# Kernel optimization log

Measured on AMD Instinct MI355X. Metric: run time of the kernel, lower is better.

## Reference

```python
import jax, jax.numpy as jnp
import numpy as np

N_NODES = 50000
N_EDGES = 1600000
NFEAT = 512
HIDDEN = 128
NUM_CLASSES = 40
DROPOUT = 0.5


def setup_inputs() -> dict:
    key = jax.random.key(0)
    ks = jax.random.split(key, 8)
    x = jax.random.normal(ks[0], (N_NODES, NFEAT), dtype=jnp.float32)
    edge_row = jax.random.randint(ks[1], (N_EDGES,), 0, N_NODES, dtype=jnp.int32)
    edge_col = jax.random.randint(ks[2], (N_EDGES,), 0, N_NODES, dtype=jnp.int32)
    edge_vals = jax.random.uniform(ks[3], (N_EDGES,), dtype=jnp.float32)
    # uniform(-stdv, stdv) init as in reset_parameters
    stdv1 = 1.0 / np.sqrt(HIDDEN)
    stdv2 = 1.0 / np.sqrt(NUM_CLASSES)
    W1 = jax.random.uniform(ks[4], (NFEAT, HIDDEN), dtype=jnp.float32, minval=-stdv1, maxval=stdv1)
    b1 = jax.random.uniform(ks[5], (HIDDEN,), dtype=jnp.float32, minval=-stdv1, maxval=stdv1)
    W2 = jax.random.uniform(ks[6], (HIDDEN, NUM_CLASSES), dtype=jnp.float32, minval=-stdv2, maxval=stdv2)
    b2 = jax.random.uniform(ks[7], (NUM_CLASSES,), dtype=jnp.float32, minval=-stdv2, maxval=stdv2)
    return {"x": x, "edge_row": edge_row, "edge_col": edge_col, "edge_vals": edge_vals,
            "W1": W1, "b1": b1, "W2": W2, "b2": b2}


def _spmm(edge_row, edge_col, edge_vals, support):
    # out[i] = sum_{e: row[e]==i} vals[e] * support[col[e]]  (sparse adj @ support)
    msgs = support[edge_col] * edge_vals[:, None]  # [E, F]
    return jax.ops.segment_sum(msgs, edge_row, num_segments=N_NODES)


def _dropout(x, rate, key):
    keep = 1.0 - rate
    mask = jax.random.bernoulli(key, keep, x.shape)
    return jnp.where(mask, x / keep, jnp.zeros((), x.dtype))


def reference(x, edge_row, edge_col, edge_vals, W1, b1, W2, b2):
    # layer 1: GCN conv + bias + relu + dropout (training=True)
    h = _spmm(edge_row, edge_col, edge_vals, x @ W1) + b1  # [N, H]
    h = jax.nn.relu(h)
    h = _dropout(h, DROPOUT, jax.random.key(42))
    # layer 2: GCN conv + bias + relu
    out = _spmm(edge_row, edge_col, edge_vals, h @ W2) + b2  # [N, C]
    return jax.nn.relu(out)
```

## Files before the change

### kernel.cpp

```cpp
#include <hip/hip_runtime.h>
#include <hip/hip_bf16.h>

#define N_NODES 50000
#define N_EDGES 1600000
#define NFEAT   512
#define HIDDEN  128
#define NCLASS  40

#define NBUCK 391
#define ROWS_PER_BUCKET 128
#define BUCK_PAD 4608

#define W1T_BLOCKS 256
#define GEMM1_BLOCKS 391
#define PART_T 4096
#define PART_BLOCKS 391

#define FUSED_LDS 37944

typedef short short8 __attribute__((ext_vector_type(8)));
typedef float f32x4  __attribute__((ext_vector_type(4)));

__device__ __forceinline__ unsigned short f2bu(float f) {
  __hip_bfloat16 h = __float2bfloat16(f);
  return *reinterpret_cast<unsigned short*>(&h);
}

__device__ __forceinline__ unsigned rotl32(unsigned x, int n) {
  return (x << n) | (x >> (32 - n));
}

__device__ __forceinline__ unsigned threefry_bits(unsigned x1) {
  unsigned x0 = 0u;
  const unsigned ks0 = 0u, ks1 = 42u, ks2 = 0x1BD11BDAu ^ 42u;
  x0 += ks0; x1 += ks1;
#define TFR(r) { x0 += x1; x1 = rotl32(x1, (r)); x1 ^= x0; }
  TFR(13) TFR(15) TFR(26) TFR(6)
  x0 += ks1; x1 += ks2 + 1u;
  TFR(17) TFR(29) TFR(16) TFR(24)
  x0 += ks2; x1 += ks0 + 2u;
  TFR(13) TFR(15) TFR(26) TFR(6)
  x0 += ks0; x1 += ks1 + 3u;
  TFR(17) TFR(29) TFR(16) TFR(24)
  x0 += ks1; x1 += ks2 + 4u;
  TFR(13) TFR(15) TFR(26) TFR(6)
  x0 += ks2; x1 += ks0 + 5u;
#undef TFR
  return x0 ^ x1;
}

__global__ __launch_bounds__(256) void init_w1t_kernel(
    const float* __restrict__ W1, unsigned short* __restrict__ W1T,
    int* __restrict__ gcur) {
  if (blockIdx.x < W1T_BLOCKS) {
    int id = blockIdx.x * 256 + threadIdx.x;
    int n = id & 127, k = id >> 7;
    W1T[n * NFEAT + k] = f2bu(W1[k * HIDDEN + n]);
  } else {
    int b = threadIdx.x;
    if (b < NBUCK) gcur[b] = b * BUCK_PAD;
    b += 256;
    if (b < NBUCK) gcur[b] = b * BUCK_PAD;
  }
}

__device__ __forceinline__ void gemm1_body(
    int bid, char* smem, const float* __restrict__ x,
    const unsigned short* __restrict__ W1T,
    unsigned short* __restrict__ support) {
  short8* As = (short8*)smem;
  short8* Bs = (short8*)(smem + 8192);
  const int t = threadIdx.x;
  const int lane = t & 63;
  const int w = t >> 6;
  const int quad = lane >> 4;
  const int l15 = lane & 15;
  const int node_base = bid * 128;
  const int mbase = (w >> 1) * 64;
  const int nbase = (w & 1) * 64;

  f32x4 acc[4][4] = {};

  for (int k0 = 0; k0 < NFEAT; k0 += 32) {
#pragma unroll
    for (int i = 0; i < 2; i++) {
      int lin = i * 256 + t;
      int n = lin >> 2, q = lin & 3;
      int row = node_base + n;
      if (row >= N_NODES) row = N_NODES - 1;
      const float* src = &x[(size_t)row * NFEAT + k0 + q * 8];
      float4 a = *(const float4*)src;
      float4 b = *(const float4*)(src + 4);
      short8 p;
      p[0] = (short)f2bu(a.x); p[1] = (short)f2bu(a.y);
      p[2] = (short)f2bu(a.z); p[3] = (short)f2bu(a.w);
      p[4] = (short)f2bu(b.x); p[5] = (short)f2bu(b.y);
      p[6] = (short)f2bu(b.z); p[7] = (short)f2bu(b.w);
      As[q * 128 + n] = p;
      Bs[q * 128 + n] = *(const short8*)&W1T[(size_t)n * NFEAT + k0 + q * 8];
    }
    __syncthreads();
    short8 af[4], bfr[4];
#pragma unroll
    for (int mt = 0; mt < 4; mt++)
      af[mt] = As[quad * 128 + mbase + mt * 16 + l15];
#pragma unroll
    for (int nt = 0; nt < 4; nt++)
      bfr[nt] = Bs[quad * 128 + nbase + nt * 16 + l15];
#pragma unroll
    for (int mt = 0; mt < 4; mt++)
#pragma unroll
      for (int nt = 0; nt < 4; nt++)
        acc[mt][nt] = __builtin_amdgcn_mfma_f32_16x16x32_bf16(
            af[mt], bfr[nt], acc[mt][nt], 0, 0, 0);
    __syncthreads();
  }

#pragma unroll
  for (int mt = 0; mt < 4; mt++)
#pragma unroll
    for (int nt = 0; nt < 4; nt++)
#pragma unroll
      for (int r = 0; r < 4; r++) {
        int row = node_base + mbase + mt * 16 + quad * 4 + r;
        int col = nbase + nt * 16 + l15;
        if (row < N_NODES)
          support[(size_t)row * HIDDEN + col] = f2bu(acc[mt][nt][r]);
      }
}

__device__ __forceinline__ void partition_body(
    int bid, char* smem, const int* __restrict__ erow,
    const int* __restrict__ ecol, const float* __restrict__ evals,
    int* __restrict__ gcur, uint2* __restrict__ eb) {
  uint2* sorted = (uint2*)smem;
  int* cnt   = (int*)(smem + 32768);
  int* shift = (int*)(smem + 32768 + 1564);
  int* ssc   = (int*)(smem + 32768 + 3128);
  const int t = threadIdx.x;
  const int base = bid * PART_T;

  if (t < NBUCK) cnt[t] = 0;
  if (t + 256 < NBUCK) cnt[t + 256] = 0;
  __syncthreads();

  uint2 er[16];
  unsigned short loc[16];
#pragma unroll
  for (int k = 0; k < 16; k++) {
    int idx = base + k * 256 + t;
    if (idx < N_EDGES) {
      int r = erow[idx];
      er[k].y = (unsigned)r;
      er[k].x = (unsigned)ecol[idx] | ((unsigned)f2bu(evals[idx]) << 16);
      loc[k] = (unsigned short)atomicAdd(&cnt[r >> 7], 1);
    } else {
      er[k].y = 0xffffffffu;
    }
  }
  __syncthreads();

  ssc[t] = (t < NBUCK) ? cnt[t] : 0;
  ssc[t + 256] = (t + 256 < NBUCK) ? cnt[t + 256] : 0;
  __syncthreads();
#pragma unroll
  for (int off = 1; off < 512; off <<= 1) {
    int v0 = (t >= off) ? ssc[t - off] : 0;
    int v1 = ssc[t + 256 - off];
    __syncthreads();
    ssc[t] += v0; ssc[t + 256] += v1;
    __syncthreads();
  }

  for (int b = t; b < NBUCK; b += 256) {
    int c = cnt[b];
    if (c > 0) {
      int lb = ssc[b] - c;
      int gb = atomicAdd(&gcur[b], c);
      shift[b] = gb - lb;
    }
  }
#pragma unroll
  for (int k = 0; k < 16; k++) {
    if (er[k].y != 0xffffffffu) {
      int b = (int)(er[k].y >> 7);
      sorted[ssc[b] - cnt[b] + (int)loc[k]] = er[k];
    }
  }
  __syncthreads();

  const int total = ssc[NBUCK - 1];
  for (int i = t; i < total; i += 256) {
    uint2 e = sorted[i];
    eb[shift[e.y >> 7] + i] = e;
  }
}

__global__ __launch_bounds__(256) void part_gemm1_kernel(
    const int* __restrict__ erow, const int* __restrict__ ecol,
    const float* __restrict__ evals, int* __restrict__ gcur,
    uint2* __restrict__ eb, const float* __restrict__ x,
    const unsigned short* __restrict__ W1T,
    unsigned short* __restrict__ support) {
  __shared__ char smem[FUSED_LDS];
  if (blockIdx.x < PART_BLOCKS)
    partition_body(blockIdx.x, smem, erow, ecol, evals, gcur, eb);
  else
    gemm1_body(blockIdx.x - PART_BLOCKS, smem, x, W1T, support);
}

__global__ __launch_bounds__(512) void csr_build_kernel(
    const uint2* __restrict__ eb, const int* __restrict__ gcur,
    unsigned* __restrict__ csr, int* __restrict__ rowptr,
    int* __restrict__ rowend) {
  __shared__ int cnt[ROWS_PER_BUCKET];
  __shared__ int sc[ROWS_PER_BUCKET];
  __shared__ int cur[ROWS_PER_BUCKET];
  const int t = threadIdx.x;
  const int b = blockIdx.x;
  if (t < ROWS_PER_BUCKET) cnt[t] = 0;
  __syncthreads();
  const int beg = b * BUCK_PAD;
  const int end = gcur[b];
  for (int j = beg + t; j < end; j += 512)
    atomicAdd(&cnt[eb[j].y & 127u], 1);
  __syncthreads();
  if (t < ROWS_PER_BUCKET) sc[t] = cnt[t];
  __syncthreads();
#pragma unroll
  for (int off = 1; off < ROWS_PER_BUCKET; off <<= 1) {
    int v = 0;
    if (t >= off && t < ROWS_PER_BUCKET) v = sc[t - off];
    __syncthreads();
    if (t < ROWS_PER_BUCKET) sc[t] += v;
    __syncthreads();
  }
  if (t < ROWS_PER_BUCKET) {
    int excl = sc[t] - cnt[t];
    cur[t] = excl;
    int row = b * ROWS_PER_BUCKET + t;
    if (row < N_NODES) {
      rowptr[row] = beg + excl;
      rowend[row] = beg + sc[t];
    }
  }
  __syncthreads();
  for (int j = beg + t; j < end; j += 512) {
    uint2 e = eb[j];
    int p = atomicAdd(&cur[e.y & 127u], 1);
    csr[beg + p] = e.x;
  }
}

__global__ __launch_bounds__(256) void spmm1_fused(
    const unsigned* __restrict__ csr, const int* __restrict__ rowptr,
    const int* __restrict__ rowend,
    const unsigned* __restrict__ sup,
    const float* __restrict__ b1, const float* __restrict__ W2,
    unsigned* __restrict__ h2u) {
  __shared__ float Ws[HIDDEN * NCLASS];
  __shared__ unsigned hrow[4][64];
  const int t = threadIdx.x;
#pragma unroll
  for (int i = 0; i < 20; i++) Ws[i * 256 + t] = W2[i * 256 + t];
  __syncthreads();

  const int row = blockIdx.x * 4 + (t >> 6);
  const int wv = t >> 6;
  const int lane = t & 63;
  const int beg = __builtin_amdgcn_readfirstlane(rowptr[row]);
  const int end = __builtin_amdgcn_readfirstlane(rowend[row]);
  float ax = 0.f, ay = 0.f;
  int j = beg;
  for (; j + 15 < end; j += 16) {
    unsigned ps[16];
#pragma unroll
    for (int k = 0; k < 16; k++)
      ps[k] = __builtin_amdgcn_readfirstlane(csr[j + k]);
    unsigned u[16];
#pragma unroll
    for (int k = 0; k < 16; k++)
      u[k] = sup[(size_t)(ps[k] & 0xffffu) * 64 + lane];
#pragma unroll
    for (int k = 0; k < 16; k++) {
      float v = __uint_as_float(ps[k] & 0xffff0000u);
      ax += v * __uint_as_float(u[k] << 16);
      ay += v * __uint_as_float(u[k] & 0xffff0000u);
    }
  }
  for (; j + 7 < end; j += 8) {
    unsigned ps[8];
#pragma unroll
    for (int k = 0; k < 8; k++)
      ps[k] = __builtin_amdgcn_readfirstlane(csr[j + k]);
    unsigned u[8];
#pragma unroll
    for (int k = 0; k < 8; k++)
      u[k] = sup[(size_t)(ps[k] & 0xffffu) * 64 + lane];
#pragma unroll
    for (int k = 0; k < 8; k++) {
      float v = __uint_as_float(ps[k] & 0xffff0000u);
      ax += v * __uint_as_float(u[k] << 16);
      ay += v * __uint_as_float(u[k] & 0xffff0000u);
    }
  }
  for (; j + 1 < end; j += 2) {
    unsigned p0 = __builtin_amdgcn_readfirstlane(csr[j]);
    unsigned p1 = __builtin_amdgcn_readfirstlane(csr[j + 1]);
    unsigned u0 = sup[(size_t)(p0 & 0xffffu) * 64 + lane];
    unsigned u1 = sup[(size_t)(p1 & 0xffffu) * 64 + lane];
    float v0 = __uint_as_float(p0 & 0xffff0000u);
    float v1 = __uint_as_float(p1 & 0xffff0000u);
    ax += v0 * __uint_as_float(u0 << 16) + v1 * __uint_as_float(u1 << 16);
    ay += v0 * __uint_as_float(u0 & 0xffff0000u) +
          v1 * __uint_as_float(u1 & 0xffff0000u);
  }
  if (j < end) {
    unsigned p0 = __builtin_amdgcn_readfirstlane(csr[j]);
    unsigned u0 = sup[(size_t)(p0 & 0xffffu) * 64 + lane];
    float v0 = __uint_as_float(p0 & 0xffff0000u);
    ax += v0 * __uint_as_float(u0 << 16);
    ay += v0 * __uint_as_float(u0 & 0xffff0000u);
  }
  const unsigned i0 = (unsigned)row * HIDDEN + lane * 2;
  float vx = fmaxf(ax + b1[lane * 2], 0.f);
  float vy = fmaxf(ay + b1[lane * 2 + 1], 0.f);
  vx = (threefry_bits(i0) >> 31) ? 0.f : 2.f * vx;
  vy = (threefry_bits(i0 + 1) >> 31) ? 0.f : 2.f * vy;
  hrow[wv][lane] = (unsigned)f2bu(vx) | ((unsigned)f2bu(vy) << 16);
  __syncthreads();

  float accv = 0.f;
  if (lane < NCLASS) {
#pragma unroll 8
    for (int i = 0; i < 64; i++) {
      unsigned u = hrow[wv][i];
      float h0 = __uint_as_float(u << 16);
      float h1 = __uint_as_float(u & 0xffff0000u);
      accv += h0 * Ws[(2 * i) * NCLASS + lane] +
              h1 * Ws[(2 * i + 1) * NCLASS + lane];
    }
    float other = __shfl_xor(accv, 1);
    if (!(lane & 1))
      h2u[(unsigned)row * 20 + (lane >> 1)] =
          (unsigned)f2bu(accv) | ((unsigned)f2bu(other) << 16);
  }
}

__global__ __launch_bounds__(256) void spmm2_fused(
    const unsigned* __restrict__ csr, const int* __restrict__ rowptr,
    const int* __restrict__ rowend,
    const unsigned* __restrict__ h2u,
    const float* __restrict__ b2, float* __restrict__ out) {
  const int row = blockIdx.x * 4 + (threadIdx.x >> 6);
  const int lane = threadIdx.x & 63;
  const int half = lane >> 5;
  const int il = lane & 31;
  const unsigned ilc = (il < 20) ? (unsigned)il : 19u;
  const int beg = rowptr[row], end = rowend[row];
  float ax = 0.f, ay = 0.f;
  int j = beg + half;
  for (; j + 6 < end; j += 8) {
    unsigned p[4], u[4];
#pragma unroll
    for (int k = 0; k < 4; k++) p[k] = csr[j + 2 * k];
#pragma unroll
    for (int k = 0; k < 4; k++) u[k] = h2u[(p[k] & 0xffffu) * 20 + ilc];
#pragma unroll
    for (int k = 0; k < 4; k++) {
      float v = __uint_as_float(p[k] & 0xffff0000u);
      ax += v * __uint_as_float(u[k] << 16);
      ay += v * __uint_as_float(u[k] & 0xffff0000u);
    }
  }
  for (; j + 2 < end; j += 4) {
    unsigned p0 = csr[j];
    unsigned p1 = csr[j + 2];
    unsigned u0 = h2u[(p0 & 0xffffu) * 20 + ilc];
    unsigned u1 = h2u[(p1 & 0xffffu) * 20 + ilc];
    float v0 = __uint_as_float(p0 & 0xffff0000u);
    float v1 = __uint_as_float(p1 & 0xffff0000u);
    ax += v0 * __uint_as_float(u0 << 16) + v1 * __uint_as_float(u1 << 16);
    ay += v0 * __uint_as_float(u0 & 0xffff0000u) +
          v1 * __uint_as_float(u1 & 0xffff0000u);
  }
  for (; j < end; j += 2) {
    unsigned p0 = csr[j];
    unsigned u0 = h2u[(p0 & 0xffffu) * 20 + ilc];
    float v0 = __uint_as_float(p0 & 0xffff0000u);
    ax += v0 * __uint_as_float(u0 << 16);
    ay += v0 * __uint_as_float(u0 & 0xffff0000u);
  }
  ax += __shfl_xor(ax, 32);
  ay += __shfl_xor(ay, 32);
  if (half == 0 && il < 20) {
    float2 r;
    r.x = fmaxf(ax + b2[il * 2], 0.f);
    r.y = fmaxf(ay + b2[il * 2 + 1], 0.f);
    *(float2*)&out[(unsigned)row * NCLASS + il * 2] = r;
  }
}

extern "C" void kernel_launch(void* const* d_in, const int* in_sizes, int n_in,
                              void* d_out, int out_size, void* d_ws,
                              size_t ws_size, hipStream_t stream) {
  const float* x     = (const float*)d_in[0];
  const int*   erow  = (const int*)d_in[1];
  const int*   ecol  = (const int*)d_in[2];
  const float* evals = (const float*)d_in[3];
  const float* W1    = (const float*)d_in[4];
  const float* b1    = (const float*)d_in[5];
  const float* W2    = (const float*)d_in[6];
  const float* b2    = (const float*)d_in[7];
  float* out = (float*)d_out;

  char* base = (char*)d_ws;
  unsigned short* support = (unsigned short*)base;
  uint2*          eb  = (uint2*)(base + 12800000);
  unsigned*       h2  = (unsigned*)(base + 27213824);
  unsigned short* W1T = (unsigned short*)(base + 31213824);
  unsigned*       csr = (unsigned*)(base + 31344896);
  int* rowptr = (int*)(base + 38551808);
  int* rowend = (int*)(base + 38751808);
  int* gcur   = (int*)(base + 38951808);

  init_w1t_kernel<<<W1T_BLOCKS + 1, 256, 0, stream>>>(W1, W1T, gcur);
  part_gemm1_kernel<<<PART_BLOCKS + GEMM1_BLOCKS, 256, 0, stream>>>(
      erow, ecol, evals, gcur, eb, x, W1T, support);
  csr_build_kernel<<<NBUCK, 512, 0, stream>>>(eb, gcur, csr, rowptr, rowend);
  spmm1_fused<<<N_NODES / 4, 256, 0, stream>>>(
      csr, rowptr, rowend, (const unsigned*)support, b1, W2, h2);
  spmm2_fused<<<N_NODES / 4, 256, 0, stream>>>(csr, rowptr, rowend,
                                               (const unsigned*)h2, b2, out);
}
```

Baseline: 313.3 us.

## Co-schedule GEMM1 with CSR build instead of partition; unpack hidden row to fp32

The edge partition step now runs as its own kernel, and GEMM1 blocks are fused with the CSR build kernel instead, which runs at 256 threads per block. Pairing GEMM1 with the lighter CSR build lowers that kernel's LDS footprint to 16KB, which may raise occupancy for the MFMA GEMM. The partition no longer overlaps with anything. Separately, spmm1 stores the dropped-out hidden row as fp32 in LDS and fully unrolls the W2 dot product, removing per-iteration bf16 unpacking.

```diff
diff --git a/kernel.cpp b/kernel.cpp
--- a/kernel.cpp
+++ b/kernel.cpp
@@ -15,8 +15,6 @@
 #define GEMM1_BLOCKS 391
 #define PART_T 4096
 #define PART_BLOCKS 391
-
-#define FUSED_LDS 37944
 
 typedef short short8 __attribute__((ext_vector_type(8)));
 typedef float f32x4  __attribute__((ext_vector_type(4)));
@@ -64,6 +62,73 @@
   }
 }
 
+__global__ __launch_bounds__(256) void partition_kernel(
+    const int* __restrict__ erow, const int* __restrict__ ecol,
+    const float* __restrict__ evals, int* __restrict__ gcur,
+    uint2* __restrict__ eb) {
+  __shared__ uint2 sorted[PART_T];
+  __shared__ int cnt[NBUCK];
+  __shared__ int shift[NBUCK];
+  __shared__ int ssc[512];
+  const int t = threadIdx.x;
+  const int base = blockIdx.x * PART_T;
+
+  if (t < NBUCK) cnt[t] = 0;
+  if (t + 256 < NBUCK) cnt[t + 256] = 0;
+  __syncthreads();
+
+  uint2 er[16];
+  unsigned short loc[16];
+#pragma unroll
+  for (int k = 0; k < 16; k++) {
+    int idx = base + k * 256 + t;
+    if (idx < N_EDGES) {
+      int r = erow[idx];
+      er[k].y = (unsigned)r;
+      er[k].x = (unsigned)ecol[idx] | ((unsigned)f2bu(evals[idx]) << 16);
+      loc[k] = (unsigned short)atomicAdd(&cnt[r >> 7], 1);
+    } else {
+      er[k].y = 0xffffffffu;
+    }
+  }
+  __syncthreads();
+
+  ssc[t] = (t < NBUCK) ? cnt[t] : 0;
+  ssc[t + 256] = (t + 256 < NBUCK) ? cnt[t + 256] : 0;
+  __syncthreads();
+#pragma unroll
+  for (int off = 1; off < 512; off <<= 1) {
+    int v0 = (t >= off) ? ssc[t - off] : 0;
+    int v1 = ssc[t + 256 - off];
+    __syncthreads();
+    ssc[t] += v0; ssc[t + 256] += v1;
+    __syncthreads();
+  }
+
+  for (int b = t; b < NBUCK; b += 256) {
+    int c = cnt[b];
+    if (c > 0) {
+      int lb = ssc[b] - c;
+      int gb = atomicAdd(&gcur[b], c);
+      shift[b] = gb - lb;
+    }
+  }
+#pragma unroll
+  for (int k = 0; k < 16; k++) {
+    if (er[k].y != 0xffffffffu) {
+      int b = (int)(er[k].y >> 7);
+      sorted[ssc[b] - cnt[b] + (int)loc[k]] = er[k];
+    }
+  }
+  __syncthreads();
+
+  const int total = ssc[NBUCK - 1];
+  for (int i = t; i < total; i += 256) {
+    uint2 e = sorted[i];
+    eb[shift[e.y >> 7] + i] = e;
+  }
+}
+
 __device__ __forceinline__ void gemm1_body(
     int bid, char* smem, const float* __restrict__ x,
     const unsigned short* __restrict__ W1T,
@@ -129,100 +194,19 @@
       }
 }
 
-__device__ __forceinline__ void partition_body(
-    int bid, char* smem, const int* __restrict__ erow,
-    const int* __restrict__ ecol, const float* __restrict__ evals,
-    int* __restrict__ gcur, uint2* __restrict__ eb) {
-  uint2* sorted = (uint2*)smem;
-  int* cnt   = (int*)(smem + 32768);
-  int* shift = (int*)(smem + 32768 + 1564);
-  int* ssc   = (int*)(smem + 32768 + 3128);
+__device__ __forceinline__ void csr_body(
+    int b, char* smem, const uint2* __restrict__ eb,
+    const int* __restrict__ gcur, unsigned* __restrict__ csr,
+    int* __restrict__ rowptr, int* __restrict__ rowend) {
+  int* cnt = (int*)smem;
+  int* sc  = (int*)(smem + 512);
+  int* cur = (int*)(smem + 1024);
   const int t = threadIdx.x;
-  const int base = bid * PART_T;
-
-  if (t < NBUCK) cnt[t] = 0;
-  if (t + 256 < NBUCK) cnt[t + 256] = 0;
-  __syncthreads();
-
-  uint2 er[16];
-  unsigned short loc[16];
-#pragma unroll
-  for (int k = 0; k < 16; k++) {
-    int idx = base + k * 256 + t;
-    if (idx < N_EDGES) {
-      int r = erow[idx];
-      er[k].y = (unsigned)r;
-      er[k].x = (unsigned)ecol[idx] | ((unsigned)f2bu(evals[idx]) << 16);
-      loc[k] = (unsigned short)atomicAdd(&cnt[r >> 7], 1);
-    } else {
-      er[k].y = 0xffffffffu;
-    }
-  }
-  __syncthreads();
-
-  ssc[t] = (t < NBUCK) ? cnt[t] : 0;
-  ssc[t + 256] = (t + 256 < NBUCK) ? cnt[t + 256] : 0;
-  __syncthreads();
-#pragma unroll
-  for (int off = 1; off < 512; off <<= 1) {
-    int v0 = (t >= off) ? ssc[t - off] : 0;
-    int v1 = ssc[t + 256 - off];
-    __syncthreads();
-    ssc[t] += v0; ssc[t + 256] += v1;
-    __syncthreads();
-  }
-
-  for (int b = t; b < NBUCK; b += 256) {
-    int c = cnt[b];
-    if (c > 0) {
-      int lb = ssc[b] - c;
-      int gb = atomicAdd(&gcur[b], c);
-      shift[b] = gb - lb;
-    }
-  }
-#pragma unroll
-  for (int k = 0; k < 16; k++) {
-    if (er[k].y != 0xffffffffu) {
-      int b = (int)(er[k].y >> 7);
-      sorted[ssc[b] - cnt[b] + (int)loc[k]] = er[k];
-    }
-  }
-  __syncthreads();
-
-  const int total = ssc[NBUCK - 1];
-  for (int i = t; i < total; i += 256) {
-    uint2 e = sorted[i];
-    eb[shift[e.y >> 7] + i] = e;
-  }
-}
-
-__global__ __launch_bounds__(256) void part_gemm1_kernel(
-    const int* __restrict__ erow, const int* __restrict__ ecol,
-    const float* __restrict__ evals, int* __restrict__ gcur,
-    uint2* __restrict__ eb, const float* __restrict__ x,
-    const unsigned short* __restrict__ W1T,
-    unsigned short* __restrict__ support) {
-  __shared__ char smem[FUSED_LDS];
-  if (blockIdx.x < PART_BLOCKS)
-    partition_body(blockIdx.x, smem, erow, ecol, evals, gcur, eb);
-  else
-    gemm1_body(blockIdx.x - PART_BLOCKS, smem, x, W1T, support);
-}
-
-__global__ __launch_bounds__(512) void csr_build_kernel(
-    const uint2* __restrict__ eb, const int* __restrict__ gcur,
-    unsigned* __restrict__ csr, int* __restrict__ rowptr,
-    int* __restrict__ rowend) {
-  __shared__ int cnt[ROWS_PER_BUCKET];
-  __shared__ int sc[ROWS_PER_BUCKET];
-  __shared__ int cur[ROWS_PER_BUCKET];
-  const int t = threadIdx.x;
-  const int b = blockIdx.x;
   if (t < ROWS_PER_BUCKET) cnt[t] = 0;
   __syncthreads();
   const int beg = b * BUCK_PAD;
   const int end = gcur[b];
-  for (int j = beg + t; j < end; j += 512)
+  for (int j = beg + t; j < end; j += 256)
     atomicAdd(&cnt[eb[j].y & 127u], 1);
   __syncthreads();
   if (t < ROWS_PER_BUCKET) sc[t] = cnt[t];
@@ -245,11 +229,24 @@
     }
   }
   __syncthreads();
-  for (int j = beg + t; j < end; j += 512) {
+  for (int j = beg + t; j < end; j += 256) {
     uint2 e = eb[j];
     int p = atomicAdd(&cur[e.y & 127u], 1);
     csr[beg + p] = e.x;
   }
+}
+
+__global__ __launch_bounds__(256) void csr_gemm1_kernel(
+    const uint2* __restrict__ eb, const int* __restrict__ gcur,
+    unsigned* __restrict__ csr, int* __restrict__ rowptr,
+    int* __restrict__ rowend, const float* __restrict__ x,
+    const unsigned short* __restrict__ W1T,
+    unsigned short* __restrict__ support) {
+  __shared__ char smem[16384];
+  if (blockIdx.x < NBUCK)
+    csr_body(blockIdx.x, smem, eb, gcur, csr, rowptr, rowend);
+  else
+    gemm1_body(blockIdx.x - NBUCK, smem, x, W1T, support);
 }
 
 __global__ __launch_bounds__(256) void spmm1_fused(
@@ -259,7 +256,7 @@
     const float* __restrict__ b1, const float* __restrict__ W2,
     unsigned* __restrict__ h2u) {
   __shared__ float Ws[HIDDEN * NCLASS];
-  __shared__ unsigned hrow[4][64];
+  __shared__ float hrowf[4][HIDDEN];
   const int t = threadIdx.x;
 #pragma unroll
   for (int i = 0; i < 20; i++) Ws[i * 256 + t] = W2[i * 256 + t];
@@ -327,19 +324,15 @@
   float vy = fmaxf(ay + b1[lane * 2 + 1], 0.f);
   vx = (threefry_bits(i0) >> 31) ? 0.f : 2.f * vx;
   vy = (threefry_bits(i0 + 1) >> 31) ? 0.f : 2.f * vy;
-  hrow[wv][lane] = (unsigned)f2bu(vx) | ((unsigned)f2bu(vy) << 16);
+  hrowf[wv][lane * 2] = __uint_as_float((unsigned)f2bu(vx) << 16);
+  hrowf[wv][lane * 2 + 1] = __uint_as_float((unsigned)f2bu(vy) << 16);
   __syncthreads();
 
   float accv = 0.f;
   if (lane < NCLASS) {
-#pragma unroll 8
-    for (int i = 0; i < 64; i++) {
-      unsigned u = hrow[wv][i];
-      float h0 = __uint_as_float(u << 16);
-      float h1 = __uint_as_float(u & 0xffff0000u);
-      accv += h0 * Ws[(2 * i) * NCLASS + lane] +
-              h1 * Ws[(2 * i + 1) * NCLASS + lane];
-    }
+#pragma unroll
+    for (int i = 0; i < HIDDEN; i++)
+      accv += hrowf[wv][i] * Ws[i * NCLASS + lane];
     float other = __shfl_xor(accv, 1);
     if (!(lane & 1))
       h2u[(unsigned)row * 20 + (lane >> 1)] =
@@ -425,9 +418,10 @@
   int* gcur   = (int*)(base + 38951808);
 
   init_w1t_kernel<<<W1T_BLOCKS + 1, 256, 0, stream>>>(W1, W1T, gcur);
-  part_gemm1_kernel<<<PART_BLOCKS + GEMM1_BLOCKS, 256, 0, stream>>>(
-      erow, ecol, evals, gcur, eb, x, W1T, support);
-  csr_build_kernel<<<NBUCK, 512, 0, stream>>>(eb, gcur, csr, rowptr, rowend);
+  partition_kernel<<<PART_BLOCKS, 256, 0, stream>>>(erow, ecol, evals, gcur,
+                                                    eb);
+  csr_gemm1_kernel<<<NBUCK + GEMM1_BLOCKS, 256, 0, stream>>>(
+      eb, gcur, csr, rowptr, rowend, x, W1T, support);
   spmm1_fused<<<N_NODES / 4, 256, 0, stream>>>(
       csr, rowptr, rowend, (const unsigned*)support, b1, W2, h2);
   spmm2_fused<<<N_NODES / 4, 256, 0, stream>>>(csr, rowptr, rowend,
```

New measurement: 320.3 us. +2.2%, slower.
